# Performance work log

Measured on AMD Instinct MI355X. Metric: run time of the kernel, lower is better.

Reference implementation:

```python
import jax, jax.numpy as jnp
import numpy as np

N_NODES = 100000


def _gcn_conv(x, W, b, src, dst, n):
    # PyG GCNConv: h = x @ W; add self-loops; norm = d^-1/2[src] * d^-1/2[dst];
    # out[i] = sum_{(s->i)} norm * h[s] + b
    h = x @ W  # [N, F_out]
    deg = jax.ops.segment_sum(jnp.ones_like(dst, dtype=h.dtype), dst, num_segments=n)
    dis = jnp.where(deg > 0, jax.lax.rsqrt(jnp.maximum(deg, 1.0)), 0.0)
    norm = dis[src] * dis[dst]  # [E]
    msg = h[src] * norm[:, None]  # [E, F_out] gather + scale
    out = jax.ops.segment_sum(msg, dst, num_segments=n)  # scatter-add
    return out + b


def _add_self_loops(edge_index, n):
    loops = jnp.arange(n, dtype=edge_index.dtype)
    src = jnp.concatenate([edge_index[0], loops])
    dst = jnp.concatenate([edge_index[1], loops])
    return src, dst


def setup_inputs() -> dict:
    key = jax.random.key(0)
    k_x, k_e, k_w1, k_w2 = jax.random.split(key, 4)
    n, e, f_in, f_hid = N_NODES, 1600000, 128, 64
    x = jax.random.normal(k_x, (n, f_in), dtype=jnp.float32)
    edge_index = jax.random.randint(k_e, (2, e), 0, n, dtype=jnp.int64)
    # Glorot-ish init for weights
    W1 = jax.random.normal(k_w1, (f_in, f_hid), dtype=jnp.float32) / np.sqrt(f_in)
    b1 = jnp.zeros((f_hid,), dtype=jnp.float32)
    W2 = jax.random.normal(k_w2, (f_hid, f_hid), dtype=jnp.float32) / np.sqrt(f_hid)
    b2 = jnp.zeros((f_hid,), dtype=jnp.float32)
    return {"x": x, "edge_index": edge_index, "W1": W1, "b1": b1, "W2": W2, "b2": b2}


def reference(x, edge_index, W1, b1, W2, b2):
    n = x.shape[0]
    src, dst = _add_self_loops(edge_index, n)
    h = jax.nn.relu(_gcn_conv(x, W1, b1, src, dst, n))
    # F.dropout(training=False) in eval mode is identity
    out = _gcn_conv(h, W2, b2, src, dst, n)
    return out
```

## Files before the change

### kernel.cpp

```cpp
#include <hip/hip_runtime.h>
#include <hip/hip_bf16.h>


#define FOUT 64
#define BW 128
#define BSH 7
#define MAXB 1024
#define CHUNK 4096
#define SLAB 3072

#define NT1 1024
#define NT2 512
#define LCOLN 2048

__device__ __forceinline__ float bf2f(unsigned int u16) {
    union { unsigned int i; float f; } c;
    c.i = u16 << 16;
    return c.f;
}
__device__ __forceinline__ unsigned short f2bf(float f) {
    union { float f; unsigned int i; } c;
    c.f = f;
    unsigned int i = c.i;
    return (unsigned short)((i + 0x7FFFu + ((i >> 16) & 1u)) >> 16);
}

typedef __attribute__((ext_vector_type(8))) short short8v;
typedef __attribute__((ext_vector_type(4))) float f32x4;

__device__ __forceinline__ void split_frag(const float* xa, short8v* Ah, short8v* Al) {
    union { unsigned int u[4]; short8v v; } H, L;
#pragma unroll
    for (int p = 0; p < 4; p++) {
        unsigned short h0 = f2bf(xa[2 * p]);
        unsigned short h1 = f2bf(xa[2 * p + 1]);
        H.u[p] = (unsigned int)h0 | ((unsigned int)h1 << 16);
        unsigned short l0 = f2bf(xa[2 * p] - bf2f(h0));
        unsigned short l1 = f2bf(xa[2 * p + 1] - bf2f(h1));
        L.u[p] = (unsigned int)l0 | ((unsigned int)l1 << 16);
    }
    *Ah = H.v;
    *Al = L.v;
}

__device__ __forceinline__ void conv_w_frag(const float* __restrict__ W,
                                            unsigned short* __restrict__ WhF,
                                            unsigned short* __restrict__ WlF,
                                            int task) {
    const int lane = task & 63;
    const int cf = (task >> 6) & 3;
    const int s = task >> 8;
    const int q = lane >> 4, m = lane & 15;
#pragma unroll
    for (int j = 0; j < 8; j++) {
        int k = s * 32 + q * 8 + j;
        float x = W[(size_t)k * 64 + cf * 16 + m];
        unsigned short h = f2bf(x);
        WhF[(size_t)task * 8 + j] = h;
        WlF[(size_t)task * 8 + j] = f2bf(x - bf2f(h));
    }
}

__global__ __launch_bounds__(512) void edge_hist(
    const int* __restrict__ dst, int* __restrict__ cnt, int E,
    const float* __restrict__ W1, const float* __restrict__ W2,
    unsigned short* __restrict__ whf1, unsigned short* __restrict__ wlf1,
    unsigned short* __restrict__ whf2, unsigned short* __restrict__ wlf2) {
    __shared__ int h[MAXB];
    const int blk = blockIdx.x, t = threadIdx.x;
    h[t] = 0;
    h[t + 512] = 0;
    __syncthreads();
    const int e0 = blk * CHUNK;
#pragma unroll
    for (int k = 0; k < CHUNK / 512; k++) {
        int e = e0 + k * 512 + t;
        if (e < E) atomicAdd(&h[dst[e] >> BSH], 1);
    }
    if (blk == 0) {
        for (int task = t; task < NT1 + NT2; task += 512) {
            if (task < NT1) conv_w_frag(W1, whf1, wlf1, task);
            else            conv_w_frag(W2, whf2, wlf2, task - NT1);
        }
    }
    __syncthreads();
    cnt[blk * MAXB + t] = h[t];
    cnt[blk * MAXB + t + 512] = h[t + 512];
}

__global__ __launch_bounds__(512) void col_scan(int* __restrict__ cnt, int nblk,
                                                int* __restrict__ gcnt) {
    __shared__ int ts[512];
    const int b = blockIdx.x;
    const int t = threadIdx.x;
    int v = (t < nblk) ? cnt[t * MAXB + b] : 0;
    ts[t] = v;
    __syncthreads();
    for (int off = 1; off < 512; off <<= 1) {
        int x = (t >= off) ? ts[t - off] : 0;
        __syncthreads();
        ts[t] += x;
        __syncthreads();
    }
    if (t < nblk) cnt[t * MAXB + b] = b * SLAB + ts[t] - v;
    if (t == 511) gcnt[b] = ts[511];
}

__global__ __launch_bounds__(512) void edge_place(
    const int* __restrict__ src, const int* __restrict__ dst,
    const int* __restrict__ cnt, int* __restrict__ ebuf, int E) {
    __shared__ int lbase[MAXB];
    __shared__ int cur[MAXB];
    const int blk = blockIdx.x, t = threadIdx.x;
    lbase[t] = cnt[blk * MAXB + t];
    lbase[t + 512] = cnt[blk * MAXB + t + 512];
    cur[t] = 0;
    cur[t + 512] = 0;
    __syncthreads();
    const int e0 = blk * CHUNK;
#pragma unroll
    for (int k = 0; k < CHUNK / 512; k++) {
        int e = e0 + k * 512 + t;
        if (e < E) {
            int d = dst[e];
            int b = d >> BSH;
            int r = atomicAdd(&cur[b], 1);
            ebuf[lbase[b] + r] = src[e] | ((d & (BW - 1)) << 17);
        }
    }
}

__global__ __launch_bounds__(256) void csr_gemm(
    int* __restrict__ ebuf, const int* __restrict__ gcnt,
    unsigned int* __restrict__ rowinfo, float* __restrict__ dis, int n,
    const float* __restrict__ X, const unsigned short* __restrict__ WhF,
    const unsigned short* __restrict__ WlF, unsigned short* __restrict__ HS) {
    constexpr int K = 128;
    __shared__ int ldeg[BW];
    __shared__ float sdis[BW];
    __shared__ int wtot[2];
    const int b = blockIdx.x, t = threadIdx.x;
    const int node0 = b << BSH;
    const int nn = min(BW, n - node0);
    const int ebeg = b * SLAB;

    const int lane = t & 63;
    const int wvv = t >> 6;
    const int m = lane & 15;
    const int q = lane >> 4;
    const int tile0 = wvv * 2, tile1 = wvv * 2 + 1;
    const int r0 = node0 + tile0 * 16 + m;
    const int r1 = node0 + tile1 * 16 + m;
    const bool ok0 = (r0 < n), ok1 = (r1 < n);
    const float* xp0 = X + (size_t)r0 * K + q * 8;
    const float* xp1 = X + (size_t)r1 * K + q * 8;
    const float4 zf4 = make_float4(0.f, 0.f, 0.f, 0.f);

    float4 c00 = zf4, c01 = zf4, c10 = zf4, c11 = zf4;
    if (ok0) { c00 = *(const float4*)xp0; c01 = *(const float4*)(xp0 + 4); }
    if (ok1) { c10 = *(const float4*)xp1; c11 = *(const float4*)(xp1 + 4); }

    int raw[SLAB / 256];
#pragma unroll
    for (int k = 0; k < SLAB / 256; k++) raw[k] = ebuf[ebeg + t + k * 256];

    const int cnt = gcnt[b];
    if (t < BW) ldeg[t] = 0;
    __syncthreads();

    int w[SLAB / 256];
#pragma unroll
    for (int k = 0; k < SLAB / 256; k++) {
        w[k] = (t + k * 256 < cnt) ? raw[k] : -1;
        if (w[k] >= 0) atomicAdd(&ldeg[w[k] >> 17], 1);
    }
    __syncthreads();

    int v = 0, pv = 0;
    if (t < BW) { v = ldeg[t]; pv = v; }
#pragma unroll
    for (int d = 1; d < 64; d <<= 1) {
        int x = __shfl_up(pv, d);
        if ((lane) >= d) pv += x;
    }
    if (t < BW && lane == 63) wtot[t >> 6] = pv;
    __syncthreads();
    if (t < BW && t >= 64) pv += wtot[0];
    const int ex = pv - v;
    if (t < nn) {
        rowinfo[node0 + t] = ((unsigned int)(ebeg + ex) << 8) | (unsigned int)v;
        float dv = rsqrtf((float)v + 1.0f);
        dis[node0 + t] = dv;
        sdis[t] = dv;
    } else if (t < BW) {
        sdis[t] = 0.f;
    }
    if (t < BW) ldeg[t] = ex;
    __syncthreads();
#pragma unroll
    for (int k = 0; k < SLAB / 256; k++)
        if (w[k] >= 0) {
            int r = atomicAdd(&ldeg[w[k] >> 17], 1);
            ebuf[ebeg + r] = w[k] & 0x1FFFF;
        }

    f32x4 acc0[4], acc1[4];
#pragma unroll
    for (int cf = 0; cf < 4; cf++) { acc0[cf] = (f32x4)0.f; acc1[cf] = (f32x4)0.f; }
    float4 n00, n01, n10, n11;

#define GSTEP(S)                                                                        \
    {                                                                                   \
        if ((S) + 1 < K / 32) {                                                         \
            n00 = zf4; n01 = zf4; n10 = zf4; n11 = zf4;                                 \
            if (ok0) { n00 = *(const float4*)(xp0 + ((S) + 1) * 32);                    \
                       n01 = *(const float4*)(xp0 + ((S) + 1) * 32 + 4); }              \
            if (ok1) { n10 = *(const float4*)(xp1 + ((S) + 1) * 32);                    \
                       n11 = *(const float4*)(xp1 + ((S) + 1) * 32 + 4); }              \
        }                                                                               \
        const unsigned short* wh = WhF + ((size_t)((S) * 4) * 64 + lane) * 8;           \
        const unsigned short* wl = WlF + ((size_t)((S) * 4) * 64 + lane) * 8;           \
        short8v Ah, Al;                                                                 \
        {                                                                               \
            const float xa[8] = {c00.x, c00.y, c00.z, c00.w, c01.x, c01.y, c01.z, c01.w}; \
            split_frag(xa, &Ah, &Al);                                                   \
        }                                                                               \
        _Pragma("unroll")                                                               \
        for (int cf = 0; cf < 4; cf++) {                                                \
            short8v bh = *(const short8v*)(wh + (size_t)cf * 64 * 8);                   \
            short8v bl = *(const short8v*)(wl + (size_t)cf * 64 * 8);                   \
            acc0[cf] = __builtin_amdgcn_mfma_f32_16x16x32_bf16(Ah, bh, acc0[cf], 0, 0, 0); \
            acc0[cf] = __builtin_amdgcn_mfma_f32_16x16x32_bf16(Al, bh, acc0[cf], 0, 0, 0); \
            acc0[cf] = __builtin_amdgcn_mfma_f32_16x16x32_bf16(Ah, bl, acc0[cf], 0, 0, 0); \
        }                                                                               \
        {                                                                               \
            const float xa[8] = {c10.x, c10.y, c10.z, c10.w, c11.x, c11.y, c11.z, c11.w}; \
            split_frag(xa, &Ah, &Al);                                                   \
        }                                                                               \
        _Pragma("unroll")                                                               \
        for (int cf = 0; cf < 4; cf++) {                                                \
            short8v bh = *(const short8v*)(wh + (size_t)cf * 64 * 8);                   \
            short8v bl = *(const short8v*)(wl + (size_t)cf * 64 * 8);                   \
            acc1[cf] = __builtin_amdgcn_mfma_f32_16x16x32_bf16(Ah, bh, acc1[cf], 0, 0, 0); \
            acc1[cf] = __builtin_amdgcn_mfma_f32_16x16x32_bf16(Al, bh, acc1[cf], 0, 0, 0); \
            acc1[cf] = __builtin_amdgcn_mfma_f32_16x16x32_bf16(Ah, bl, acc1[cf], 0, 0, 0); \
        }                                                                               \
        c00 = n00; c01 = n01; c10 = n10; c11 = n11;                                     \
    }
    GSTEP(0) GSTEP(1) GSTEP(2) GSTEP(3)
#undef GSTEP

#pragma unroll
    for (int r = 0; r < 4; r++) {
        int row = node0 + tile0 * 16 + q * 4 + r;
        if (row < n) {
            float dr = sdis[tile0 * 16 + q * 4 + r];
#pragma unroll
            for (int cf = 0; cf < 4; cf++)
                HS[(size_t)row * FOUT + cf * 16 + m] = f2bf(acc0[cf][r] * dr);
        }
        row = node0 + tile1 * 16 + q * 4 + r;
        if (row < n) {
            float dr = sdis[tile1 * 16 + q * 4 + r];
#pragma unroll
            for (int cf = 0; cf < 4; cf++)
                HS[(size_t)row * FOUT + cf * 16 + m] = f2bf(acc1[cf][r] * dr);
        }
    }
}

__device__ __forceinline__ void acc8(const uint4 u, float* a) {
    a[0] += bf2f(u.x & 0xFFFFu); a[1] += bf2f(u.x >> 16);
    a[2] += bf2f(u.y & 0xFFFFu); a[3] += bf2f(u.y >> 16);
    a[4] += bf2f(u.z & 0xFFFFu); a[5] += bf2f(u.z >> 16);
    a[6] += bf2f(u.w & 0xFFFFu); a[7] += bf2f(u.w >> 16);
}

__device__ __forceinline__ void stage_cols(
    const unsigned int* __restrict__ rowinfo, const int* __restrict__ col,
    int* lcol, int* sbs, int i0, int n, int tid) {
    if (tid == 0) {
        int last = min(i0 + 31, n - 1);
        unsigned int r0 = rowinfo[i0];
        unsigned int rl = rowinfo[last];
        int base = (int)(r0 >> 8);
        sbs[0] = base;
        sbs[1] = (int)(rl >> 8) + (int)(rl & 255u) - base;
    }
    __syncthreads();
    const int span = sbs[1];
    if (span <= LCOLN) {
        const int base = sbs[0];
        for (int k = tid; k < span; k += 256) lcol[k] = col[base + k];
    }
    __syncthreads();
}

#define OSTR 68
__global__ __launch_bounds__(256) void agg_gemm(
    const uint4* __restrict__ hsv, const unsigned int* __restrict__ rowinfo,
    const int* __restrict__ col, const float* __restrict__ dis,
    const float* __restrict__ bias,
    const unsigned short* __restrict__ WhF2, const unsigned short* __restrict__ WlF2,
    unsigned short* __restrict__ HS2, int n) {
    __shared__ float so[32 * OSTR];
    __shared__ int lcol[LCOLN];
    __shared__ int sbs[2];
    const int tid = threadIdx.x;
    const int wv = tid >> 6;
    const int lane = tid & 63;
    const int g = lane >> 3;
    const int jj = lane & 7;
    const int lrow = wv * 8 + g;
    const int i0 = blockIdx.x * 32;
    const int i = i0 + lrow;

    const unsigned int info = (i < n) ? rowinfo[i] : 0u;
    uint4 su = make_uint4(0u, 0u, 0u, 0u);
    if (i < n) su = hsv[(size_t)i * 8 + jj];

    stage_cols(rowinfo, col, lcol, sbs, i0, n, tid);
    const int base = sbs[0], span = sbs[1];
    const bool uselds = (span <= LCOLN);

    float o[8];
#pragma unroll
    for (int p = 0; p < 8; p++) o[p] = 0.f;

    if (i < n) {
        const int beg = (int)(info >> 8);
        const int deg = (int)(info & 255u);
        const int off = beg - base;

        float a[8];
        a[0] = bf2f(su.x & 0xFFFFu); a[1] = bf2f(su.x >> 16);
        a[2] = bf2f(su.y & 0xFFFFu); a[3] = bf2f(su.y >> 16);
        a[4] = bf2f(su.z & 0xFFFFu); a[5] = bf2f(su.z >> 16);
        a[6] = bf2f(su.w & 0xFFFFu); a[7] = bf2f(su.w >> 16);

        int qq = 0;
        for (; qq + 4 <= deg; qq += 4) {
            int s0 = uselds ? lcol[off + qq]     : col[beg + qq];
            int s1 = uselds ? lcol[off + qq + 1] : col[beg + qq + 1];
            int s2 = uselds ? lcol[off + qq + 2] : col[beg + qq + 2];
            int s3 = uselds ? lcol[off + qq + 3] : col[beg + qq + 3];
            uint4 u0 = hsv[(size_t)s0 * 8 + jj];
            uint4 u1 = hsv[(size_t)s1 * 8 + jj];
            uint4 u2 = hsv[(size_t)s2 * 8 + jj];
            uint4 u3 = hsv[(size_t)s3 * 8 + jj];
            acc8(u0, a); acc8(u1, a); acc8(u2, a); acc8(u3, a);
        }
        for (; qq < deg; qq++) {
            int s = uselds ? lcol[off + qq] : col[beg + qq];
            acc8(hsv[(size_t)s * 8 + jj], a);
        }
        float d = dis[i];
        const float4* b4 = (const float4*)bias;
        float4 bb0 = b4[jj * 2];
        float4 bb1 = b4[jj * 2 + 1];
        o[0] = fmaxf(d * a[0] + bb0.x, 0.f);
        o[1] = fmaxf(d * a[1] + bb0.y, 0.f);
        o[2] = fmaxf(d * a[2] + bb0.z, 0.f);
        o[3] = fmaxf(d * a[3] + bb0.w, 0.f);
        o[4] = fmaxf(d * a[4] + bb1.x, 0.f);
        o[5] = fmaxf(d * a[5] + bb1.y, 0.f);
        o[6] = fmaxf(d * a[6] + bb1.z, 0.f);
        o[7] = fmaxf(d * a[7] + bb1.w, 0.f);
    }
    {
        float* sp = &so[lrow * OSTR + jj * 8];
        *(float4*)sp = make_float4(o[0], o[1], o[2], o[3]);
        *(float4*)(sp + 4) = make_float4(o[4], o[5], o[6], o[7]);
    }
    __syncthreads();

    const int tile = wv >> 1;
    const int ch = wv & 1;
    const int m = lane & 15;
    const int q = lane >> 4;
    f32x4 acc[2];
    acc[0] = (f32x4)0.f;
    acc[1] = (f32x4)0.f;
#pragma unroll
    for (int s = 0; s < 2; s++) {
        const float* ap = &so[(tile * 16 + m) * OSTR + s * 32 + q * 8];
        float4 v0 = *(const float4*)ap;
        float4 v1 = *(const float4*)(ap + 4);
        const float xa[8] = {v0.x, v0.y, v0.z, v0.w, v1.x, v1.y, v1.z, v1.w};
        short8v Ah, Al;
        split_frag(xa, &Ah, &Al);
#pragma unroll
        for (int c = 0; c < 2; c++) {
            int cf = ch * 2 + c;
            const unsigned short* wh = WhF2 + ((size_t)(s * 4 + cf) * 64 + lane) * 8;
            const unsigned short* wl = WlF2 + ((size_t)(s * 4 + cf) * 64 + lane) * 8;
            short8v bh = *(const short8v*)wh;
            short8v bl = *(const short8v*)wl;
            acc[c] = __builtin_amdgcn_mfma_f32_16x16x32_bf16(Ah, bh, acc[c], 0, 0, 0);
            acc[c] = __builtin_amdgcn_mfma_f32_16x16x32_bf16(Al, bh, acc[c], 0, 0, 0);
            acc[c] = __builtin_amdgcn_mfma_f32_16x16x32_bf16(Ah, bl, acc[c], 0, 0, 0);
        }
    }
#pragma unroll
    for (int r = 0; r < 4; r++) {
        int lr = tile * 16 + q * 4 + r;
        int i2 = blockIdx.x * 32 + lr;
        if (i2 < n) {
            float dr = dis[i2];
#pragma unroll
            for (int c = 0; c < 2; c++) {
                HS2[(size_t)i2 * FOUT + (ch * 2 + c) * 16 + m] = f2bf(acc[c][r] * dr);
            }
        }
    }
}

template <bool RELU>
__global__ __launch_bounds__(256) void aggregate(
    const uint4* __restrict__ hsv, const unsigned int* __restrict__ rowinfo,
    const int* __restrict__ col, const float* __restrict__ dis,
    const float* __restrict__ bias, float* __restrict__ out, int n) {
    __shared__ int lcol[LCOLN];
    __shared__ int sbs[2];
    const int tid = threadIdx.x;
    const int wv = tid >> 6;
    const int lane = tid & 63;
    const int g = lane >> 3;
    const int jj = lane & 7;
    const int i0 = blockIdx.x * 32;
    const int i = i0 + wv * 8 + g;

    const unsigned int info = (i < n) ? rowinfo[i] : 0u;
    uint4 su = make_uint4(0u, 0u, 0u, 0u);
    if (i < n) su = hsv[(size_t)i * 8 + jj];

    stage_cols(rowinfo, col, lcol, sbs, i0, n, tid);
    const int base = sbs[0], span = sbs[1];
    const bool uselds = (span <= LCOLN);

    if (i >= n) return;

    const int beg = (int)(info >> 8);
    const int deg = (int)(info & 255u);
    const int off = beg - base;

    float a[8];
    a[0] = bf2f(su.x & 0xFFFFu); a[1] = bf2f(su.x >> 16);
    a[2] = bf2f(su.y & 0xFFFFu); a[3] = bf2f(su.y >> 16);
    a[4] = bf2f(su.z & 0xFFFFu); a[5] = bf2f(su.z >> 16);
    a[6] = bf2f(su.w & 0xFFFFu); a[7] = bf2f(su.w >> 16);

    int qq = 0;
    for (; qq + 4 <= deg; qq += 4) {
        int s0 = uselds ? lcol[off + qq]     : col[beg + qq];
        int s1 = uselds ? lcol[off + qq + 1] : col[beg + qq + 1];
        int s2 = uselds ? lcol[off + qq + 2] : col[beg + qq + 2];
        int s3 = uselds ? lcol[off + qq + 3] : col[beg + qq + 3];
        uint4 u0 = hsv[(size_t)s0 * 8 + jj];
        uint4 u1 = hsv[(size_t)s1 * 8 + jj];
        uint4 u2 = hsv[(size_t)s2 * 8 + jj];
        uint4 u3 = hsv[(size_t)s3 * 8 + jj];
        acc8(u0, a); acc8(u1, a); acc8(u2, a); acc8(u3, a);
    }
    for (; qq < deg; qq++) {
        int s = uselds ? lcol[off + qq] : col[beg + qq];
        acc8(hsv[(size_t)s * 8 + jj], a);
    }
    float d = dis[i];
    const float4* b4 = (const float4*)bias;
    float4 bb0 = b4[jj * 2];
    float4 bb1 = b4[jj * 2 + 1];
    float4 o0, o1;
    o0.x = d * a[0] + bb0.x; o0.y = d * a[1] + bb0.y;
    o0.z = d * a[2] + bb0.z; o0.w = d * a[3] + bb0.w;
    o1.x = d * a[4] + bb1.x; o1.y = d * a[5] + bb1.y;
    o1.z = d * a[6] + bb1.z; o1.w = d * a[7] + bb1.w;
    if (RELU) {
        o0.x = fmaxf(o0.x, 0.f); o0.y = fmaxf(o0.y, 0.f);
        o0.z = fmaxf(o0.z, 0.f); o0.w = fmaxf(o0.w, 0.f);
        o1.x = fmaxf(o1.x, 0.f); o1.y = fmaxf(o1.y, 0.f);
        o1.z = fmaxf(o1.z, 0.f); o1.w = fmaxf(o1.w, 0.f);
    }
    float4* orow = (float4*)out + (size_t)i * 16 + jj * 2;
    orow[0] = o0;
    orow[1] = o1;
}

extern "C" void kernel_launch(void* const* d_in, const int* in_sizes, int n_in,
                              void* d_out, int out_size, void* d_ws, size_t ws_size,
                              hipStream_t stream) {
    const float* x  = (const float*)d_in[0];
    const int*   ei = (const int*)d_in[1];
    const float* W1 = (const float*)d_in[2];
    const float* b1 = (const float*)d_in[3];
    const float* W2 = (const float*)d_in[4];
    const float* b2 = (const float*)d_in[5];

    const int n = in_sizes[0] / 128;
    const int E = in_sizes[1] / 2;
    const int* srcp = ei;
    const int* dstp = ei + E;

    float* out = (float*)d_out;

    const int B = (n + BW - 1) / BW;
    const int nblk = (E + CHUNK - 1) / CHUNK;

    int*            cnt     = (int*)d_ws;
    int*            gcnt    = cnt + 512 * MAXB;
    unsigned int*   rowinfo = (unsigned int*)(gcnt + MAXB);
    float*          dis     = (float*)(rowinfo + n);
    int*            ebuf    = (int*)(dis + n);
    unsigned short* hs      = (unsigned short*)(ebuf + (size_t)B * SLAB);
    unsigned short* whf1    = hs + (size_t)n * FOUT;
    unsigned short* wlf1    = whf1 + (size_t)NT1 * 8;
    unsigned short* whf2    = wlf1 + (size_t)NT1 * 8;
    unsigned short* wlf2    = whf2 + (size_t)NT2 * 8;
    unsigned short* hs2     = wlf2 + (size_t)NT2 * 8;

    edge_hist<<<nblk, 512, 0, stream>>>(dstp, cnt, E, W1, W2,
                                        whf1, wlf1, whf2, wlf2);
    col_scan<<<B, 512, 0, stream>>>(cnt, nblk, gcnt);
    edge_place<<<nblk, 512, 0, stream>>>(srcp, dstp, cnt, ebuf, E);

    csr_gemm<<<B, 256, 0, stream>>>(ebuf, gcnt, rowinfo, dis, n,
                                    x, whf1, wlf1, hs);

    agg_gemm<<<(n + 31) / 32, 256, 0, stream>>>(
        (const uint4*)hs, rowinfo, ebuf, dis, b1, whf2, wlf2, hs2, n);

    aggregate<false><<<(n + 31) / 32, 256, 0, stream>>>(
        (const uint4*)hs2, rowinfo, ebuf, dis, b2, out, n);
}
```

Measured before the change: 217.5 us.

## Fuse CSR build and first GEMM into one persistent kernel with grid barriers

Merges the histogram, column scan, edge placement and CSR/GEMM kernels into a single launch of B blocks, one per node bucket. The blocks synchronise through global atomic spin barriers, and the edge chunk size is adjusted so that one block covers each bucket's share of edges. This removes three kernel launches and keeps the dst indices in registers between phases. It also relies on all B (~782) blocks being co-resident; if they are not, the spin barriers deadlock, and the spinning adds its own latency.

```diff
diff --git a/kernel.cpp b/kernel.cpp
--- a/kernel.cpp
+++ b/kernel.cpp
@@ -6,7 +6,7 @@
 #define BW 128
 #define BSH 7
 #define MAXB 1024
-#define CHUNK 4096
+#define CHUNK2 2048
 #define SLAB 3072
 
 #define NT1 1024
@@ -27,6 +27,20 @@
 
 typedef __attribute__((ext_vector_type(8))) short short8v;
 typedef __attribute__((ext_vector_type(4))) float f32x4;
+
+__device__ __forceinline__ void gbar(int* __restrict__ bar, int idx, int nB,
+                                     int tid) {
+    __threadfence();
+    __syncthreads();
+    if (tid == 0) {
+        atomicAdd(&bar[idx], 1);
+        while (__hip_atomic_load(&bar[idx], __ATOMIC_RELAXED,
+                                 __HIP_MEMORY_SCOPE_AGENT) < nB)
+            __builtin_amdgcn_s_sleep(8);
+    }
+    __syncthreads();
+    __threadfence();
+}
 
 __device__ __forceinline__ void split_frag(const float* xa, short8v* Ah, short8v* Al) {
     union { unsigned int u[4]; short8v v; } H, L;
@@ -61,132 +75,137 @@
     }
 }
 
-__global__ __launch_bounds__(512) void edge_hist(
-    const int* __restrict__ dst, int* __restrict__ cnt, int E,
+__global__ __launch_bounds__(256, 4) void csr_all(
+    const int* __restrict__ src, const int* __restrict__ dst, int E,
+    int* __restrict__ bar, int* __restrict__ cnt, int* __restrict__ ebuf,
+    unsigned int* __restrict__ rowinfo, float* __restrict__ dis, int n,
+    const float* __restrict__ X,
     const float* __restrict__ W1, const float* __restrict__ W2,
     unsigned short* __restrict__ whf1, unsigned short* __restrict__ wlf1,
-    unsigned short* __restrict__ whf2, unsigned short* __restrict__ wlf2) {
-    __shared__ int h[MAXB];
-    const int blk = blockIdx.x, t = threadIdx.x;
-    h[t] = 0;
-    h[t + 512] = 0;
-    __syncthreads();
-    const int e0 = blk * CHUNK;
-#pragma unroll
-    for (int k = 0; k < CHUNK / 512; k++) {
-        int e = e0 + k * 512 + t;
-        if (e < E) atomicAdd(&h[dst[e] >> BSH], 1);
-    }
-    if (blk == 0) {
-        for (int task = t; task < NT1 + NT2; task += 512) {
+    unsigned short* __restrict__ whf2, unsigned short* __restrict__ wlf2,
+    unsigned short* __restrict__ HS) {
+    __shared__ int shA[MAXB];
+    __shared__ int shB[MAXB];
+    __shared__ float sdis[BW];
+    __shared__ int wtot[4];
+    __shared__ int btot;
+
+    const int g = blockIdx.x, t = threadIdx.x;
+    const int nB = gridDim.x;
+    const int lane = t & 63, wv = t >> 6;
+    const int node0 = g << BSH;
+
+    int edst[CHUNK2 / 256];
+    const int e0 = g * CHUNK2;
+#pragma unroll
+    for (int k = 0; k < CHUNK2 / 256; k++) {
+        int e = e0 + k * 256 + t;
+        edst[k] = (e < E) ? dst[e] : -1;
+    }
+#pragma unroll
+    for (int k = 0; k < MAXB / 256; k++) shA[t + 256 * k] = 0;
+    __syncthreads();
+#pragma unroll
+    for (int k = 0; k < CHUNK2 / 256; k++)
+        if (edst[k] >= 0) atomicAdd(&shA[edst[k] >> BSH], 1);
+    if (g == 0) {
+        for (int task = t; task < NT1 + NT2; task += 256) {
             if (task < NT1) conv_w_frag(W1, whf1, wlf1, task);
             else            conv_w_frag(W2, whf2, wlf2, task - NT1);
         }
     }
     __syncthreads();
-    cnt[blk * MAXB + t] = h[t];
-    cnt[blk * MAXB + t + 512] = h[t + 512];
-}
-
-__global__ __launch_bounds__(512) void col_scan(int* __restrict__ cnt, int nblk,
-                                                int* __restrict__ gcnt) {
-    __shared__ int ts[512];
-    const int b = blockIdx.x;
-    const int t = threadIdx.x;
-    int v = (t < nblk) ? cnt[t * MAXB + b] : 0;
-    ts[t] = v;
-    __syncthreads();
-    for (int off = 1; off < 512; off <<= 1) {
-        int x = (t >= off) ? ts[t - off] : 0;
-        __syncthreads();
-        ts[t] += x;
-        __syncthreads();
-    }
-    if (t < nblk) cnt[t * MAXB + b] = b * SLAB + ts[t] - v;
-    if (t == 511) gcnt[b] = ts[511];
-}
-
-__global__ __launch_bounds__(512) void edge_place(
-    const int* __restrict__ src, const int* __restrict__ dst,
-    const int* __restrict__ cnt, int* __restrict__ ebuf, int E) {
-    __shared__ int lbase[MAXB];
-    __shared__ int cur[MAXB];
-    const int blk = blockIdx.x, t = threadIdx.x;
-    lbase[t] = cnt[blk * MAXB + t];
-    lbase[t + 512] = cnt[blk * MAXB + t + 512];
-    cur[t] = 0;
-    cur[t + 512] = 0;
-    __syncthreads();
-    const int e0 = blk * CHUNK;
-#pragma unroll
-    for (int k = 0; k < CHUNK / 512; k++) {
-        int e = e0 + k * 512 + t;
-        if (e < E) {
-            int d = dst[e];
-            int b = d >> BSH;
-            int r = atomicAdd(&cur[b], 1);
-            ebuf[lbase[b] + r] = src[e] | ((d & (BW - 1)) << 17);
-        }
-    }
-}
-
-__global__ __launch_bounds__(256) void csr_gemm(
-    int* __restrict__ ebuf, const int* __restrict__ gcnt,
-    unsigned int* __restrict__ rowinfo, float* __restrict__ dis, int n,
-    const float* __restrict__ X, const unsigned short* __restrict__ WhF,
-    const unsigned short* __restrict__ WlF, unsigned short* __restrict__ HS) {
-    constexpr int K = 128;
-    __shared__ int ldeg[BW];
-    __shared__ float sdis[BW];
-    __shared__ int wtot[2];
-    const int b = blockIdx.x, t = threadIdx.x;
-    const int node0 = b << BSH;
-    const int nn = min(BW, n - node0);
-    const int ebeg = b * SLAB;
-
-    const int lane = t & 63;
-    const int wvv = t >> 6;
+#pragma unroll
+    for (int k = 0; k < MAXB / 256; k++) cnt[g * MAXB + t + 256 * k] = shA[t + 256 * k];
+    gbar(bar, 0, nB, t);
+
+    int aa[4];
+#pragma unroll
+    for (int i = 0; i < 4; i++) {
+        int j = 4 * t + i;
+        aa[i] = (j < nB) ? cnt[j * MAXB + g] : 0;
+    }
+    int s = aa[0] + aa[1] + aa[2] + aa[3];
+    int pv = s;
+#pragma unroll
+    for (int d = 1; d < 64; d <<= 1) {
+        int x = __shfl_up(pv, d);
+        if (lane >= d) pv += x;
+    }
+    if (lane == 63) wtot[wv] = pv;
+    __syncthreads();
+    int woff = 0;
+#pragma unroll
+    for (int ww = 0; ww < 4; ww++)
+        if (ww < wv) woff += wtot[ww];
+    int run = woff + pv - s;
+#pragma unroll
+    for (int i = 0; i < 4; i++) {
+        int j = 4 * t + i;
+        if (j < nB) cnt[j * MAXB + g] = g * SLAB + run;
+        run += aa[i];
+    }
+    if (t == 0) btot = wtot[0] + wtot[1] + wtot[2] + wtot[3];
+    gbar(bar, 1, nB, t);
+
+    int sv[CHUNK2 / 256];
+#pragma unroll
+    for (int k = 0; k < CHUNK2 / 256; k++)
+        sv[k] = (edst[k] >= 0) ? src[e0 + k * 256 + t] : 0;
+#pragma unroll
+    for (int k = 0; k < MAXB / 256; k++) {
+        shA[t + 256 * k] = cnt[g * MAXB + t + 256 * k];
+        shB[t + 256 * k] = 0;
+    }
+    __syncthreads();
+#pragma unroll
+    for (int k = 0; k < CHUNK2 / 256; k++)
+        if (edst[k] >= 0) {
+            int bb = edst[k] >> BSH;
+            int r = atomicAdd(&shB[bb], 1);
+            ebuf[shA[bb] + r] = sv[k] | ((edst[k] & (BW - 1)) << 17);
+        }
+    gbar(bar, 2, nB, t);
+
     const int m = lane & 15;
     const int q = lane >> 4;
-    const int tile0 = wvv * 2, tile1 = wvv * 2 + 1;
+    const int tile0 = wv * 2, tile1 = wv * 2 + 1;
     const int r0 = node0 + tile0 * 16 + m;
     const int r1 = node0 + tile1 * 16 + m;
     const bool ok0 = (r0 < n), ok1 = (r1 < n);
-    const float* xp0 = X + (size_t)r0 * K + q * 8;
-    const float* xp1 = X + (size_t)r1 * K + q * 8;
+    const float* xp0 = X + (size_t)r0 * 128 + q * 8;
+    const float* xp1 = X + (size_t)r1 * 128 + q * 8;
     const float4 zf4 = make_float4(0.f, 0.f, 0.f, 0.f);
-
     float4 c00 = zf4, c01 = zf4, c10 = zf4, c11 = zf4;
     if (ok0) { c00 = *(const float4*)xp0; c01 = *(const float4*)(xp0 + 4); }
     if (ok1) { c10 = *(const float4*)xp1; c11 = *(const float4*)(xp1 + 4); }
 
+    const int nn = min(BW, n - node0);
+    const int ebeg = g * SLAB;
     int raw[SLAB / 256];
 #pragma unroll
     for (int k = 0; k < SLAB / 256; k++) raw[k] = ebuf[ebeg + t + k * 256];
-
-    const int cnt = gcnt[b];
-    if (t < BW) ldeg[t] = 0;
-    __syncthreads();
-
+    const int cntE = btot;
+    if (t < BW) shB[t] = 0;
+    __syncthreads();
     int w[SLAB / 256];
 #pragma unroll
     for (int k = 0; k < SLAB / 256; k++) {
-        w[k] = (t + k * 256 < cnt) ? raw[k] : -1;
-        if (w[k] >= 0) atomicAdd(&ldeg[w[k] >> 17], 1);
-    }
-    __syncthreads();
-
-    int v = 0, pv = 0;
-    if (t < BW) { v = ldeg[t]; pv = v; }
+        w[k] = (t + k * 256 < cntE) ? raw[k] : -1;
+        if (w[k] >= 0) atomicAdd(&shB[w[k] >> 17], 1);
+    }
+    __syncthreads();
+    int v = 0, pv2 = 0;
+    if (t < BW) { v = shB[t]; pv2 = v; }
 #pragma unroll
     for (int d = 1; d < 64; d <<= 1) {
-        int x = __shfl_up(pv, d);
-        if ((lane) >= d) pv += x;
-    }
-    if (t < BW && lane == 63) wtot[t >> 6] = pv;
-    __syncthreads();
-    if (t < BW && t >= 64) pv += wtot[0];
-    const int ex = pv - v;
+        int x = __shfl_up(pv2, d);
+        if (lane >= d) pv2 += x;
+    }
+    if (t < BW && lane == 63) wtot[t >> 6] = pv2;
+    __syncthreads();
+    if (t < BW && t >= 64) pv2 += wtot[0];
+    const int ex = pv2 - v;
     if (t < nn) {
         rowinfo[node0 + t] = ((unsigned int)(ebeg + ex) << 8) | (unsigned int)v;
         float dv = rsqrtf((float)v + 1.0f);
@@ -195,12 +214,12 @@
     } else if (t < BW) {
         sdis[t] = 0.f;
     }
-    if (t < BW) ldeg[t] = ex;
+    if (t < BW) shB[t] = ex;
     __syncthreads();
 #pragma unroll
     for (int k = 0; k < SLAB / 256; k++)
         if (w[k] >= 0) {
-            int r = atomicAdd(&ldeg[w[k] >> 17], 1);
+            int r = atomicAdd(&shB[w[k] >> 17], 1);
             ebuf[ebeg + r] = w[k] & 0x1FFFF;
         }
 
@@ -211,15 +230,15 @@
 
 #define GSTEP(S)                                                                        \
     {                                                                                   \
-        if ((S) + 1 < K / 32) {                                                         \
+        if ((S) + 1 < 4) {                                                              \
             n00 = zf4; n01 = zf4; n10 = zf4; n11 = zf4;                                 \
             if (ok0) { n00 = *(const float4*)(xp0 + ((S) + 1) * 32);                    \
                        n01 = *(const float4*)(xp0 + ((S) + 1) * 32 + 4); }              \
             if (ok1) { n10 = *(const float4*)(xp1 + ((S) + 1) * 32);                    \
                        n11 = *(const float4*)(xp1 + ((S) + 1) * 32 + 4); }              \
         }                                                                               \
-        const unsigned short* wh = WhF + ((size_t)((S) * 4) * 64 + lane) * 8;           \
-        const unsigned short* wl = WlF + ((size_t)((S) * 4) * 64 + lane) * 8;           \
+        const unsigned short* wh = whf1 + ((size_t)((S) * 4) * 64 + lane) * 8;          \
+        const unsigned short* wl = wlf1 + ((size_t)((S) * 4) * 64 + lane) * 8;          \
         short8v Ah, Al;                                                                 \
         {                                                                               \
             const float xa[8] = {c00.x, c00.y, c00.z, c00.w, c01.x, c01.y, c01.z, c01.w}; \
@@ -504,11 +523,10 @@
     float* out = (float*)d_out;
 
     const int B = (n + BW - 1) / BW;
-    const int nblk = (E + CHUNK - 1) / CHUNK;
-
-    int*            cnt     = (int*)d_ws;
-    int*            gcnt    = cnt + 512 * MAXB;
-    unsigned int*   rowinfo = (unsigned int*)(gcnt + MAXB);
+
+    int*            bar     = (int*)d_ws;
+    int*            cnt     = bar + 64;
+    unsigned int*   rowinfo = (unsigned int*)(cnt + (size_t)MAXB * MAXB);
     float*          dis     = (float*)(rowinfo + n);
     int*            ebuf    = (int*)(dis + n);
     unsigned short* hs      = (unsigned short*)(ebuf + (size_t)B * SLAB);
@@ -518,13 +536,11 @@
     unsigned short* wlf2    = whf2 + (size_t)NT2 * 8;
     unsigned short* hs2     = wlf2 + (size_t)NT2 * 8;
 
-    edge_hist<<<nblk, 512, 0, stream>>>(dstp, cnt, E, W1, W2,
-                                        whf1, wlf1, whf2, wlf2);
-    col_scan<<<B, 512, 0, stream>>>(cnt, nblk, gcnt);
-    edge_place<<<nblk, 512, 0, stream>>>(srcp, dstp, cnt, ebuf, E);
-
-    csr_gemm<<<B, 256, 0, stream>>>(ebuf, gcnt, rowinfo, dis, n,
-                                    x, whf1, wlf1, hs);
+    hipMemsetAsync(bar, 0, 64 * sizeof(int), stream);
+
+    csr_all<<<B, 256, 0, stream>>>(srcp, dstp, E, bar, cnt, ebuf, rowinfo,
+                                   dis, n, x, W1, W2, whf1, wlf1, whf2, wlf2,
+                                   hs);
 
     agg_gemm<<<(n + 31) / 32, 256, 0, stream>>>(
         (const uint4*)hs, rowinfo, ebuf, dis, b1, whf2, wlf2, hs2, n);
```

After: 768.3 us. +253.2%, slower.
